# Kernel tuning notes

Measured on AMD Instinct MI355X. Metric: run time of the kernel, lower is better.

## Reference

```python
import jax, jax.numpy as jnp
import numpy as np
from jax import lax

B, T, C_IN, HID, K, HORIZON = 64, 1024, 256, 512, 3, 12
OUT_DIM = HORIZON * 3


def causal_conv(x, w, b, dilation):
    # x: (B, C_in, T), w: (C_out, C_in, K) -> left-padded causal conv == conv+Chomp1d
    pad = (K - 1) * dilation
    y = lax.conv_general_dilated(x, w, window_strides=(1,), padding=[(pad, 0)],
                                 rhs_dilation=(dilation,),
                                 dimension_numbers=('NCH', 'OIH', 'NCH'))
    return y + b[None, :, None]


def setup_inputs() -> dict:
    key = jax.random.key(0)
    ks = jax.random.split(key, 16)
    N = B * T
    x = jax.random.normal(ks[0], (N, C_IN), jnp.float32)
    edge_index = jax.random.randint(ks[1], (2, N), 0, N, dtype=jnp.int64)
    idx = jnp.arange(N, dtype=jnp.int64)
    batch = idx // T          # graph id per node
    node_time = idx % T       # local time per node
    s1 = 1.0 / np.sqrt(C_IN * K)
    s2 = 1.0 / np.sqrt(HID * K)
    sd = 1.0 / np.sqrt(C_IN)
    sf = 1.0 / np.sqrt(HID)
    return {
        'x': x, 'edge_index': edge_index, 'batch': batch, 'node_time': node_time,
        # TemporalBlock 0 (in=C_IN, out=HID, dilation=1)
        'conv1_w0': jax.random.uniform(ks[2], (HID, C_IN, K), jnp.float32, -s1, s1),
        'conv1_b0': jax.random.uniform(ks[3], (HID,), jnp.float32, -s1, s1),
        'conv2_w0': jax.random.uniform(ks[4], (HID, HID, K), jnp.float32, -s2, s2),
        'conv2_b0': jax.random.uniform(ks[5], (HID,), jnp.float32, -s2, s2),
        'down_w0': jax.random.uniform(ks[6], (HID, C_IN, 1), jnp.float32, -sd, sd),
        'down_b0': jax.random.uniform(ks[7], (HID,), jnp.float32, -sd, sd),
        # TemporalBlock 1 (in=HID, out=HID, dilation=2, no downsample)
        'conv1_w1': jax.random.uniform(ks[8], (HID, HID, K), jnp.float32, -s2, s2),
        'conv1_b1': jax.random.uniform(ks[9], (HID,), jnp.float32, -s2, s2),
        'conv2_w1': jax.random.uniform(ks[10], (HID, HID, K), jnp.float32, -s2, s2),
        'conv2_b1': jax.random.uniform(ks[11], (HID,), jnp.float32, -s2, s2),
        # fc
        'fc_w': jax.random.uniform(ks[12], (OUT_DIM, HID), jnp.float32, -sf, sf),
        'fc_b': jax.random.uniform(ks[13], (OUT_DIM,), jnp.float32, -sf, sf),
    }


def reference(x, edge_index, batch, node_time,
              conv1_w0, conv1_b0, conv2_w0, conv2_b0, down_w0, down_b0,
              conv1_w1, conv1_b1, conv2_w1, conv2_b1, fc_w, fc_b):
    # vectorized scatter replacing the per-node Python loop
    x_seq = jnp.zeros((B, T, C_IN), x.dtype).at[batch, node_time].set(x)
    h = x_seq.transpose(0, 2, 1)  # (B, C_IN, T)
    # TemporalBlock 0 (dropout inactive in eval)
    out = jax.nn.relu(causal_conv(h, conv1_w0, conv1_b0, 1))
    out = jax.nn.relu(causal_conv(out, conv2_w0, conv2_b0, 1))
    res = jnp.einsum('bct,oc->bot', h, down_w0[:, :, 0]) + down_b0[None, :, None]
    h = jax.nn.relu(out + res)
    # TemporalBlock 1
    out = jax.nn.relu(causal_conv(h, conv1_w1, conv1_b1, 2))
    out = jax.nn.relu(causal_conv(out, conv2_w1, conv2_b1, 2))
    h = jax.nn.relu(out + h)
    # last timestep -> fc
    return h[:, :, -1] @ fc_w.T + fc_b
```

## Files before the change

kernel.cpp:

```cpp
#include <hip/hip_runtime.h>


#define HIDC 512
#define OUTD 36

__global__ __launch_bounds__(256) void k_tr(const float* __restrict__ x,
                                            float* __restrict__ xT) {
    const int r = blockIdx.x, cq = blockIdx.y, tid = threadIdx.x;
    __shared__ float S[64][65];
    for (int it = 0; it < 16; ++it) {
        int i = tid + 256 * it;
        int b = i >> 6, c = i & 63;
        S[b][c] = x[(b * 1024 + 1011 + r) * 256 + cq * 64 + c];
    }
    __syncthreads();
    for (int it = 0; it < 16; ++it) {
        int i = tid + 256 * it;
        int c = i >> 6, b = i & 63;
        xT[((cq * 64 + c) * 13 + r) * 64 + b] = S[b][c];
    }
}

template <int CIN, int TIN, int TOUT, int S, int D, int OFF, int TAPS,
          int OCT, int CCH, int NCH, int P1N, int P2N>
__global__ __launch_bounds__(256) void k_conv(
    const float* __restrict__ src1, const float* __restrict__ bias1,
    const float* __restrict__ src2, const float* __restrict__ bias2,
    const float* __restrict__ w, float* __restrict__ Pout) {
    const int tid = threadIdx.x, lane = tid & 63, wv = tid >> 6;
    const int ocp = blockIdx.x, ks = blockIdx.y;
    const int oc0 = ocp * OCT;
    constexpr int OCR = OCT / 4;
    constexpr int TINP = TIN;
    __shared__ float Als[CCH * TAPS * OCT];
    __shared__ float Bls[CCH * 64 * TINP];
    float acc[OCR][TOUT];
#pragma unroll
    for (int i = 0; i < OCR; ++i)
#pragma unroll
        for (int t = 0; t < TOUT; ++t) acc[i][t] = 0.f;

    for (int ch = 0; ch < NCH; ++ch) {
        const int c0 = (ks * NCH + ch) * CCH;
        if (ch) __syncthreads();
        for (int idx = tid; idx < OCT * CCH * TAPS; idx += 256) {
            int i = idx / (CCH * TAPS), r = idx % (CCH * TAPS);
            int c = r / TAPS, kk = r % TAPS;
            Als[(c * TAPS + kk) * OCT + i] =
                w[(size_t)(oc0 + i) * (CIN * TAPS) + (c0 + c) * TAPS + kk];
        }
        for (int idx = tid; idx < CCH * TIN * 16; idx += 256) {
            int c = idx / (TIN * 16), r = idx % (TIN * 16);
            int t = r / 16, b4 = (r % 16) * 4;
            float4 v;
            if constexpr (P1N == 0) {
                v = *(const float4*)(src1 + ((size_t)(c0 + c) * TIN + t) * 64 + b4);
            } else {
                float4 s = {0.f, 0.f, 0.f, 0.f};
#pragma unroll
                for (int p = 0; p < P1N; ++p) {
                    float4 u = *(const float4*)(src1 +
                        (((size_t)p * CIN + c0 + c) * TIN + t) * 64 + b4);
                    s.x += u.x; s.y += u.y; s.z += u.z; s.w += u.w;
                }
                float bb = bias1[c0 + c];
                s.x = fmaxf(s.x + bb, 0.f); s.y = fmaxf(s.y + bb, 0.f);
                s.z = fmaxf(s.z + bb, 0.f); s.w = fmaxf(s.w + bb, 0.f);
                if constexpr (P2N > 0) {
                    float4 s2 = {0.f, 0.f, 0.f, 0.f};
#pragma unroll
                    for (int p = 0; p < P2N; ++p) {
                        float4 u = *(const float4*)(src2 +
                            (((size_t)p * CIN + c0 + c) * TIN + t) * 64 + b4);
                        s2.x += u.x; s2.y += u.y; s2.z += u.z; s2.w += u.w;
                    }
                    float b2v = bias2[c0 + c];
                    s.x = fmaxf(s.x + s2.x + b2v, 0.f);
                    s.y = fmaxf(s.y + s2.y + b2v, 0.f);
                    s.z = fmaxf(s.z + s2.z + b2v, 0.f);
                    s.w = fmaxf(s.w + s2.w + b2v, 0.f);
                }
                v = s;
            }
            Bls[(c * 64 + b4 + 0) * TINP + t] = v.x;
            Bls[(c * 64 + b4 + 1) * TINP + t] = v.y;
            Bls[(c * 64 + b4 + 2) * TINP + t] = v.z;
            Bls[(c * 64 + b4 + 3) * TINP + t] = v.w;
        }
        __syncthreads();
        for (int c = 0; c < CCH; ++c) {
            float bv[TIN];
#pragma unroll
            for (int u = 0; u < TIN; ++u) bv[u] = Bls[(c * 64 + lane) * TINP + u];
            float av[TAPS][OCR];
#pragma unroll
            for (int kk = 0; kk < TAPS; ++kk)
#pragma unroll
                for (int i = 0; i < OCR; ++i)
                    av[kk][i] = Als[(c * TAPS + kk) * OCT + wv * OCR + i];
#pragma unroll
            for (int i = 0; i < OCR; ++i)
#pragma unroll
                for (int t = 0; t < TOUT; ++t)
#pragma unroll
                    for (int kk = 0; kk < TAPS; ++kk)
                        acc[i][t] += av[kk][i] * bv[S * t + D * kk + OFF];
        }
    }
#pragma unroll
    for (int i = 0; i < OCR; ++i)
#pragma unroll
        for (int t = 0; t < TOUT; ++t)
            Pout[(((size_t)blockIdx.y * HIDC + oc0 + wv * OCR + i) * TOUT + t) * 64 +
                 lane] = acc[i][t];
}

__global__ __launch_bounds__(512) void k_fc(
    const float* __restrict__ P3, const float* __restrict__ P1,
    const float* __restrict__ PD, const float* __restrict__ b2_1,
    const float* __restrict__ b2_0, const float* __restrict__ bd0,
    const float* __restrict__ fcw, const float* __restrict__ fcb,
    float* __restrict__ out) {
    const int b = blockIdx.x, tid = threadIdx.x;
    __shared__ float H1s[HIDC];
    __shared__ float fcP[OUTD][8];
    {
        const int oc = tid;
        float s3 = 0.f, s1 = 0.f, sd = 0.f;
#pragma unroll
        for (int p = 0; p < 16; ++p) s3 += P3[((size_t)p * HIDC + oc) * 64 + b];
#pragma unroll
        for (int p = 0; p < 16; ++p)
            s1 += P1[(((size_t)p * HIDC + oc) * 5 + 4) * 64 + b];
#pragma unroll
        for (int p = 0; p < 8; ++p)
            sd += PD[(((size_t)p * HIDC + oc) * 5 + 4) * 64 + b];
        float h0 = fmaxf(fmaxf(s1 + b2_0[oc], 0.f) + sd + bd0[oc], 0.f);
        H1s[oc] = fmaxf(fmaxf(s3 + b2_1[oc], 0.f) + h0, 0.f);
    }
    __syncthreads();
    if (tid < OUTD * 8) {
        int j = tid >> 3, part = tid & 7;
        float s = 0.f;
        for (int o = part; o < HIDC; o += 8) s += fcw[j * HIDC + o] * H1s[o];
        fcP[j][part] = s;
    }
    __syncthreads();
    if (tid < OUTD) {
        float s = fcb[tid];
#pragma unroll
        for (int r = 0; r < 8; ++r) s += fcP[tid][r];
        out[b * OUTD + tid] = s;
    }
}

extern "C" void kernel_launch(void* const* d_in, const int* in_sizes, int n_in,
                              void* d_out, int out_size, void* d_ws, size_t ws_size,
                              hipStream_t stream) {
    const float* x    = (const float*)d_in[0];
    const float* w1_0 = (const float*)d_in[4];
    const float* b1_0 = (const float*)d_in[5];
    const float* w2_0 = (const float*)d_in[6];
    const float* b2_0 = (const float*)d_in[7];
    const float* wd0  = (const float*)d_in[8];
    const float* bd0  = (const float*)d_in[9];
    const float* w1_1 = (const float*)d_in[10];
    const float* b1_1 = (const float*)d_in[11];
    const float* w2_1 = (const float*)d_in[12];
    const float* b2_1 = (const float*)d_in[13];
    const float* fcw  = (const float*)d_in[14];
    const float* fcb  = (const float*)d_in[15];
    float* out = (float*)d_out;

    float* xT = (float*)d_ws;
    float* P0 = xT + 256 * 13 * 64;
    float* P1 = P0 + 8 * 512 * 11 * 64;
    float* PD = P1 + 16 * 512 * 5 * 64;
    float* P2 = PD + 8 * 512 * 5 * 64;
    float* P3 = P2 + 16 * 512 * 3 * 64;

    k_tr<<<dim3(13, 4), 256, 0, stream>>>(x, xT);
    k_conv<256, 13, 11, 1, 1, 0, 3, 16, 16, 2, 0, 0>
        <<<dim3(32, 8), 256, 0, stream>>>(xT, nullptr, nullptr, nullptr, w1_0, P0);
    k_conv<256, 13, 5, 2, 0, 4, 1, 32, 16, 2, 0, 0>
        <<<dim3(16, 8), 256, 0, stream>>>(xT, nullptr, nullptr, nullptr, wd0, PD);
    k_conv<512, 11, 5, 2, 1, 0, 3, 32, 16, 2, 8, 0>
        <<<dim3(16, 16), 256, 0, stream>>>(P0, b1_0, nullptr, nullptr, w2_0, P1);
    k_conv<512, 5, 3, 1, 1, 0, 3, 32, 32, 1, 16, 8>
        <<<dim3(16, 16), 256, 0, stream>>>(P1, b2_0, PD, bd0, w1_1, P2);
    k_conv<512, 3, 1, 1, 1, 0, 3, 32, 32, 1, 16, 0>
        <<<dim3(16, 16), 256, 0, stream>>>(P2, b1_1, nullptr, nullptr, w2_1, P3);
    k_fc<<<64, 512, 0, stream>>>(P3, P1, PD, b2_1, b2_0, bd0, fcw, fcb, out);
}
```

Before: 146.5 us.

## Split-K reductions into separate kernels and read x directly in conv stages

```diff
diff --git a/kernel.cpp b/kernel.cpp
--- a/kernel.cpp
+++ b/kernel.cpp
@@ -1,39 +1,18 @@
 #include <hip/hip_runtime.h>
 
 
-#define HIDC 512
 #define OUTD 36
 
-__global__ __launch_bounds__(256) void k_tr(const float* __restrict__ x,
-                                            float* __restrict__ xT) {
-    const int r = blockIdx.x, cq = blockIdx.y, tid = threadIdx.x;
-    __shared__ float S[64][65];
-    for (int it = 0; it < 16; ++it) {
-        int i = tid + 256 * it;
-        int b = i >> 6, c = i & 63;
-        S[b][c] = x[(b * 1024 + 1011 + r) * 256 + cq * 64 + c];
-    }
-    __syncthreads();
-    for (int it = 0; it < 16; ++it) {
-        int i = tid + 256 * it;
-        int c = i >> 6, b = i & 63;
-        xT[((cq * 64 + c) * 13 + r) * 64 + b] = S[b][c];
-    }
-}
-
-template <int CIN, int TIN, int TOUT, int S, int D, int OFF, int TAPS,
-          int OCT, int CCH, int NCH, int P1N, int P2N>
-__global__ __launch_bounds__(256) void k_conv(
-    const float* __restrict__ src1, const float* __restrict__ bias1,
-    const float* __restrict__ src2, const float* __restrict__ bias2,
-    const float* __restrict__ w, float* __restrict__ Pout) {
+template <int CIN, int TS_N, int TP, int TOUT, int S, int D, int OFF, int TAPS,
+          int OCT, int CCH, int NCH, bool SRC_X, int TS_BASE, int TS_STEP>
+__global__ __launch_bounds__(256) void k_conv(const float* __restrict__ src,
+                                              const float* __restrict__ w,
+                                              float* __restrict__ Pout) {
     const int tid = threadIdx.x, lane = tid & 63, wv = tid >> 6;
-    const int ocp = blockIdx.x, ks = blockIdx.y;
-    const int oc0 = ocp * OCT;
+    const int oc0 = blockIdx.x * OCT;
     constexpr int OCR = OCT / 4;
-    constexpr int TINP = TIN;
     __shared__ float Als[CCH * TAPS * OCT];
-    __shared__ float Bls[CCH * 64 * TINP];
+    __shared__ float Bls[CCH * 64 * TP];
     float acc[OCR][TOUT];
 #pragma unroll
     for (int i = 0; i < OCR; ++i)
@@ -41,7 +20,7 @@
         for (int t = 0; t < TOUT; ++t) acc[i][t] = 0.f;
 
     for (int ch = 0; ch < NCH; ++ch) {
-        const int c0 = (ks * NCH + ch) * CCH;
+        const int c0 = (blockIdx.y * NCH + ch) * CCH;
         if (ch) __syncthreads();
         for (int idx = tid; idx < OCT * CCH * TAPS; idx += 256) {
             int i = idx / (CCH * TAPS), r = idx % (CCH * TAPS);
@@ -49,55 +28,41 @@
             Als[(c * TAPS + kk) * OCT + i] =
                 w[(size_t)(oc0 + i) * (CIN * TAPS) + (c0 + c) * TAPS + kk];
         }
-        for (int idx = tid; idx < CCH * TIN * 16; idx += 256) {
-            int c = idx / (TIN * 16), r = idx % (TIN * 16);
-            int t = r / 16, b4 = (r % 16) * 4;
-            float4 v;
-            if constexpr (P1N == 0) {
-                v = *(const float4*)(src1 + ((size_t)(c0 + c) * TIN + t) * 64 + b4);
+        if constexpr (SRC_X) {
+            for (int idx = tid; idx < CCH * TS_N * 64; idx += 256) {
+                int c = idx % CCH, rb = idx / CCH;
+                int b = rb & 63, u = rb >> 6;
+                Bls[(c * 64 + b) * TP + u] =
+                    src[((size_t)b * 1024 + 1011 + TS_BASE + TS_STEP * u) * 256 +
+                        c0 + c];
+            }
+        } else {
+            const float4* gp = (const float4*)(src + (size_t)c0 * 64 * TP);
+            float4* lp = (float4*)Bls;
+            for (int idx = tid; idx < CCH * 64 * TP / 4; idx += 256)
+                lp[idx] = gp[idx];
+        }
+        __syncthreads();
+        constexpr int NLOAD = (TP % 4 == 0) ? TP : TS_N;
+        for (int c = 0; c < CCH; ++c) {
+            float bv[NLOAD];
+            if constexpr (TP % 4 == 0) {
+#pragma unroll
+                for (int q = 0; q < TP / 4; ++q)
+                    *(float4*)&bv[4 * q] =
+                        *(const float4*)&Bls[(c * 64 + lane) * TP + 4 * q];
             } else {
-                float4 s = {0.f, 0.f, 0.f, 0.f};
-#pragma unroll
-                for (int p = 0; p < P1N; ++p) {
-                    float4 u = *(const float4*)(src1 +
-                        (((size_t)p * CIN + c0 + c) * TIN + t) * 64 + b4);
-                    s.x += u.x; s.y += u.y; s.z += u.z; s.w += u.w;
-                }
-                float bb = bias1[c0 + c];
-                s.x = fmaxf(s.x + bb, 0.f); s.y = fmaxf(s.y + bb, 0.f);
-                s.z = fmaxf(s.z + bb, 0.f); s.w = fmaxf(s.w + bb, 0.f);
-                if constexpr (P2N > 0) {
-                    float4 s2 = {0.f, 0.f, 0.f, 0.f};
-#pragma unroll
-                    for (int p = 0; p < P2N; ++p) {
-                        float4 u = *(const float4*)(src2 +
-                            (((size_t)p * CIN + c0 + c) * TIN + t) * 64 + b4);
-                        s2.x += u.x; s2.y += u.y; s2.z += u.z; s2.w += u.w;
-                    }
-                    float b2v = bias2[c0 + c];
-                    s.x = fmaxf(s.x + s2.x + b2v, 0.f);
-                    s.y = fmaxf(s.y + s2.y + b2v, 0.f);
-                    s.z = fmaxf(s.z + s2.z + b2v, 0.f);
-                    s.w = fmaxf(s.w + s2.w + b2v, 0.f);
-                }
-                v = s;
+#pragma unroll
+                for (int u = 0; u < TS_N; ++u)
+                    bv[u] = Bls[(c * 64 + lane) * TP + u];
             }
-            Bls[(c * 64 + b4 + 0) * TINP + t] = v.x;
-            Bls[(c * 64 + b4 + 1) * TINP + t] = v.y;
-            Bls[(c * 64 + b4 + 2) * TINP + t] = v.z;
-            Bls[(c * 64 + b4 + 3) * TINP + t] = v.w;
-        }
-        __syncthreads();
-        for (int c = 0; c < CCH; ++c) {
-            float bv[TIN];
-#pragma unroll
-            for (int u = 0; u < TIN; ++u) bv[u] = Bls[(c * 64 + lane) * TINP + u];
             float av[TAPS][OCR];
 #pragma unroll
             for (int kk = 0; kk < TAPS; ++kk)
 #pragma unroll
-                for (int i = 0; i < OCR; ++i)
-                    av[kk][i] = Als[(c * TAPS + kk) * OCT + wv * OCR + i];
+                for (int j = 0; j < OCR; j += 4)
+                    *(float4*)&av[kk][j] =
+                        *(const float4*)&Als[(c * TAPS + kk) * OCT + wv * OCR + j];
 #pragma unroll
             for (int i = 0; i < OCR; ++i)
 #pragma unroll
@@ -111,47 +76,81 @@
     for (int i = 0; i < OCR; ++i)
 #pragma unroll
         for (int t = 0; t < TOUT; ++t)
-            Pout[(((size_t)blockIdx.y * HIDC + oc0 + wv * OCR + i) * TOUT + t) * 64 +
+            Pout[(((size_t)blockIdx.y * 512 + oc0 + wv * OCR + i) * TOUT + t) * 64 +
                  lane] = acc[i][t];
 }
 
-__global__ __launch_bounds__(512) void k_fc(
-    const float* __restrict__ P3, const float* __restrict__ P1,
-    const float* __restrict__ PD, const float* __restrict__ b2_1,
-    const float* __restrict__ b2_0, const float* __restrict__ bd0,
-    const float* __restrict__ fcw, const float* __restrict__ fcb,
-    float* __restrict__ out) {
-    const int b = blockIdx.x, tid = threadIdx.x;
-    __shared__ float H1s[HIDC];
-    __shared__ float fcP[OUTD][8];
-    {
-        const int oc = tid;
-        float s3 = 0.f, s1 = 0.f, sd = 0.f;
-#pragma unroll
-        for (int p = 0; p < 16; ++p) s3 += P3[((size_t)p * HIDC + oc) * 64 + b];
-#pragma unroll
-        for (int p = 0; p < 16; ++p)
-            s1 += P1[(((size_t)p * HIDC + oc) * 5 + 4) * 64 + b];
-#pragma unroll
-        for (int p = 0; p < 8; ++p)
-            sd += PD[(((size_t)p * HIDC + oc) * 5 + 4) * 64 + b];
-        float h0 = fmaxf(fmaxf(s1 + b2_0[oc], 0.f) + sd + bd0[oc], 0.f);
-        H1s[oc] = fmaxf(fmaxf(s3 + b2_1[oc], 0.f) + h0, 0.f);
-    }
-    __syncthreads();
-    if (tid < OUTD * 8) {
-        int j = tid >> 3, part = tid & 7;
-        float s = 0.f;
-        for (int o = part; o < HIDC; o += 8) s += fcw[j * HIDC + o] * H1s[o];
-        fcP[j][part] = s;
-    }
-    __syncthreads();
-    if (tid < OUTD) {
-        float s = fcb[tid];
-#pragma unroll
-        for (int r = 0; r < 8; ++r) s += fcP[tid][r];
-        out[b * OUTD + tid] = s;
-    }
+template <int KS1, int T, int TPo, int KS2, bool RES>
+__global__ __launch_bounds__(256) void k_red(const float* __restrict__ P1,
+                                             const float* __restrict__ bias1,
+                                             const float* __restrict__ P2,
+                                             const float* __restrict__ bias2,
+                                             const float* __restrict__ res,
+                                             float* __restrict__ outp) {
+    const int oc = blockIdx.x, tid = threadIdx.x;
+    __shared__ float Sm[64 * TPo];
+    if constexpr (TPo > 1) {
+        for (int i = tid; i < 64 * TPo; i += 256) Sm[i] = 0.f;
+        __syncthreads();
+    }
+    if (tid < T * 16) {
+        const int t = tid / 16, b4 = (tid % 16) * 4;
+        float4 s = make_float4(0.f, 0.f, 0.f, 0.f);
+#pragma unroll
+        for (int p = 0; p < KS1; ++p) {
+            float4 u =
+                *(const float4*)(P1 + (((size_t)p * 512 + oc) * T + t) * 64 + b4);
+            s.x += u.x; s.y += u.y; s.z += u.z; s.w += u.w;
+        }
+        const float b1 = bias1[oc];
+        s.x = fmaxf(s.x + b1, 0.f); s.y = fmaxf(s.y + b1, 0.f);
+        s.z = fmaxf(s.z + b1, 0.f); s.w = fmaxf(s.w + b1, 0.f);
+        if constexpr (KS2 > 0) {
+            float4 s2 = make_float4(0.f, 0.f, 0.f, 0.f);
+#pragma unroll
+            for (int p = 0; p < KS2; ++p) {
+                float4 u =
+                    *(const float4*)(P2 + (((size_t)p * 512 + oc) * T + t) * 64 + b4);
+                s2.x += u.x; s2.y += u.y; s2.z += u.z; s2.w += u.w;
+            }
+            const float b2v = bias2[oc];
+            s.x = fmaxf(s.x + s2.x + b2v, 0.f);
+            s.y = fmaxf(s.y + s2.y + b2v, 0.f);
+            s.z = fmaxf(s.z + s2.z + b2v, 0.f);
+            s.w = fmaxf(s.w + s2.w + b2v, 0.f);
+        }
+        if constexpr (RES) {
+            s.x = fmaxf(s.x + res[((size_t)oc * 64 + b4 + 0) * 12 + 4], 0.f);
+            s.y = fmaxf(s.y + res[((size_t)oc * 64 + b4 + 1) * 12 + 4], 0.f);
+            s.z = fmaxf(s.z + res[((size_t)oc * 64 + b4 + 2) * 12 + 4], 0.f);
+            s.w = fmaxf(s.w + res[((size_t)oc * 64 + b4 + 3) * 12 + 4], 0.f);
+        }
+        if constexpr (TPo == 1) {
+            *(float4*)(outp + (size_t)oc * 64 + b4) = s;
+        } else {
+            Sm[(b4 + 0) * TPo + t] = s.x;
+            Sm[(b4 + 1) * TPo + t] = s.y;
+            Sm[(b4 + 2) * TPo + t] = s.z;
+            Sm[(b4 + 3) * TPo + t] = s.w;
+        }
+    }
+    if constexpr (TPo > 1) {
+        __syncthreads();
+        float4* op = (float4*)(outp + (size_t)oc * 64 * TPo);
+        for (int i = tid; i < 64 * TPo / 4; i += 256)
+            op[i] = *(const float4*)&Sm[4 * i];
+    }
+}
+
+__global__ __launch_bounds__(64) void k_fc(const float* __restrict__ H1,
+                                           const float* __restrict__ fcw,
+                                           const float* __restrict__ fcb,
+                                           float* __restrict__ out) {
+    const int j = blockIdx.x, lane = threadIdx.x;
+    float acc = fcb[j];
+#pragma unroll 8
+    for (int o = 0; o < 512; ++o) acc += fcw[j * 512 + o] * H1[o * 64 + lane];
+    out[lane * OUTD + j] = acc;
 }
 
 extern "C" void kernel_launch(void* const* d_in, const int* in_sizes, int n_in,
@@ -172,23 +171,33 @@
     const float* fcb  = (const float*)d_in[15];
     float* out = (float*)d_out;
 
-    float* xT = (float*)d_ws;
-    float* P0 = xT + 256 * 13 * 64;
-    float* P1 = P0 + 8 * 512 * 11 * 64;
-    float* PD = P1 + 16 * 512 * 5 * 64;
-    float* P2 = PD + 8 * 512 * 5 * 64;
-    float* P3 = P2 + 16 * 512 * 3 * 64;
-
-    k_tr<<<dim3(13, 4), 256, 0, stream>>>(x, xT);
-    k_conv<256, 13, 11, 1, 1, 0, 3, 16, 16, 2, 0, 0>
-        <<<dim3(32, 8), 256, 0, stream>>>(xT, nullptr, nullptr, nullptr, w1_0, P0);
-    k_conv<256, 13, 5, 2, 0, 4, 1, 32, 16, 2, 0, 0>
-        <<<dim3(16, 8), 256, 0, stream>>>(xT, nullptr, nullptr, nullptr, wd0, PD);
-    k_conv<512, 11, 5, 2, 1, 0, 3, 32, 16, 2, 8, 0>
-        <<<dim3(16, 16), 256, 0, stream>>>(P0, b1_0, nullptr, nullptr, w2_0, P1);
-    k_conv<512, 5, 3, 1, 1, 0, 3, 32, 32, 1, 16, 8>
-        <<<dim3(16, 16), 256, 0, stream>>>(P1, b2_0, PD, bd0, w1_1, P2);
-    k_conv<512, 3, 1, 1, 1, 0, 3, 32, 32, 1, 16, 0>
-        <<<dim3(16, 16), 256, 0, stream>>>(P2, b1_1, nullptr, nullptr, w2_1, P3);
-    k_fc<<<64, 512, 0, stream>>>(P3, P1, PD, b2_1, b2_0, bd0, fcw, fcb, out);
-}
+    float* P0  = (float*)d_ws;
+    float* B1  = P0 + 8 * 512 * 11 * 64;
+    float* P1  = B1 + 512 * 64 * 12;
+    float* PD  = P1 + 16 * 512 * 5 * 64;
+    float* H0  = PD + 8 * 512 * 5 * 64;
+    float* P2  = H0 + 512 * 64 * 12;
+    float* B2  = P2 + 16 * 512 * 3 * 64;
+    float* P3  = B2 + 512 * 64 * 4;
+    float* H1g = P3 + 8 * 512 * 64;
+
+    k_conv<256, 13, 13, 11, 1, 1, 0, 3, 16, 16, 2, true, 0, 1>
+        <<<dim3(32, 8), 256, 0, stream>>>(x, w1_0, P0);
+    k_conv<256, 5, 5, 5, 1, 0, 0, 1, 32, 16, 2, true, 4, 2>
+        <<<dim3(16, 8), 256, 0, stream>>>(x, wd0, PD);
+    k_red<8, 11, 12, 0, false><<<512, 256, 0, stream>>>(P0, b1_0, nullptr,
+                                                        nullptr, nullptr, B1);
+    k_conv<512, 11, 12, 5, 2, 1, 0, 3, 32, 16, 2, false, 0, 0>
+        <<<dim3(16, 16), 256, 0, stream>>>(B1, w2_0, P1);
+    k_red<16, 5, 12, 8, false><<<512, 256, 0, stream>>>(P1, b2_0, PD, bd0,
+                                                        nullptr, H0);
+    k_conv<512, 5, 12, 3, 1, 1, 0, 3, 32, 16, 2, false, 0, 0>
+        <<<dim3(16, 16), 256, 0, stream>>>(H0, w1_1, P2);
+    k_red<16, 3, 4, 0, false><<<512, 256, 0, stream>>>(P2, b1_1, nullptr,
+                                                       nullptr, nullptr, B2);
+    k_conv<512, 3, 4, 1, 1, 1, 0, 3, 32, 32, 2, false, 0, 0>
+        <<<dim3(16, 8), 256, 0, stream>>>(B2, w2_1, P3);
+    k_red<8, 1, 1, 0, true><<<512, 256, 0, stream>>>(P3, b2_1, nullptr, nullptr,
+                                                     H0, H1g);
+    k_fc<<<OUTD, 64, 0, stream>>>(H1g, fcw, fcb, out);
+}
```

Result: faster. 125.0 us (-14.7%).
